# Performance work log

Hardware: AMD Instinct MI355X
Metric: run time of the kernel (lower is better)

Reference implementation:

```python
import jax, jax.numpy as jnp
import numpy as np

N, F, H, K, T, O = 4096, 64, 64, 2, 5, 32  # nodes, in_feat, hidden, heads, temporal_steps, out


def setup_inputs() -> dict:
    key = jax.random.key(0)
    ks = jax.random.split(key, 12)
    s = 0.05
    return {
        "node_features": jax.random.normal(ks[0], (N, F), jnp.float32),
        "adj_matrix": jax.random.randint(ks[1], (N, N), 0, 2, jnp.int32),
        "temporal_features": jax.random.normal(ks[2], (N, T, H), jnp.float32),
        # GAT params (stacked over K heads). Linear W: Wh = h @ W.T, so W_gat[k] is [H, F].
        "W_gat": jax.random.normal(ks[3], (K, H, F), jnp.float32) * s,
        "a_src": jax.random.normal(ks[4], (K, H), jnp.float32) * s,  # first half of a (repeat -> column/neighbor index)
        "a_dst": jax.random.normal(ks[5], (K, H), jnp.float32) * s,  # second half of a (repeat_interleave -> row/self index)
        # LSTM (1 layer, input K*H, hidden H), PyTorch gate order i,f,g,o
        "W_ih": jax.random.normal(ks[6], (4 * H, K * H), jnp.float32) * s,
        "W_hh": jax.random.normal(ks[7], (4 * H, H), jnp.float32) * s,
        "b_ih": jax.random.normal(ks[8], (4 * H,), jnp.float32) * s,
        "b_hh": jax.random.normal(ks[9], (4 * H,), jnp.float32) * s,
        # fc
        "fc_W": jax.random.normal(ks[10], (O, H), jnp.float32) * s,
        "fc_b": jax.random.normal(ks[11], (O,), jnp.float32) * s,
    }


def reference(node_features, adj_matrix, temporal_features,
              W_gat, a_src, a_dst, W_ih, W_hh, b_ih, b_hh, fc_W, fc_b):
    # ---- GAT heads (vectorized over K) ----
    Wh = jnp.einsum("nf,khf->knh", node_features, W_gat)          # [K,N,H]
    # a([Wh_i, Wh_j]) == a_src.Wh_j + a_dst.Wh_i; e[p,q] = lrelu(dst[p] + src[q])
    s_src = jnp.einsum("knh,kh->kn", Wh, a_src)                    # column term
    s_dst = jnp.einsum("knh,kh->kn", Wh, a_dst)                    # row term
    e = jax.nn.leaky_relu(s_dst[:, :, None] + s_src[:, None, :], 0.2)  # [K,N,N]
    e = jnp.where(adj_matrix[None, :, :] > 0, e, jnp.float32(-1e9))
    att = jax.nn.softmax(e, axis=-1)                               # dropout = identity (eval)
    h_prime = jax.nn.elu(jnp.einsum("kpq,kqh->kph", att, Wh))      # [K,N,H]
    h = jnp.transpose(h_prime, (1, 0, 2)).reshape(N, K * H)        # concat heads [N, K*H]
    # ---- LSTM over seq of length 1 (h.unsqueeze(1)); h0 = c0 = 0 ----
    gates = h @ W_ih.T + b_ih + b_hh                               # h0 @ W_hh.T == 0
    i, f, g, o = jnp.split(gates, 4, axis=-1)
    c = jax.nn.sigmoid(i) * jnp.tanh(g)                            # f * c0 == 0
    h_t = jax.nn.sigmoid(o) * jnp.tanh(c)                          # [N,H]
    return h_t @ fc_W.T + fc_b                                     # [N,O]
```

## Files before the change

### kernel.cpp

```cpp
#include <hip/hip_runtime.h>


#define NN 4096

typedef __attribute__((ext_vector_type(8))) short bf16x8;
typedef __attribute__((ext_vector_type(4))) float f32x4;

__device__ inline unsigned short bf_rne(float f) {
    unsigned u = __float_as_uint(f);
    u += 0x7fffu + ((u >> 16) & 1u);
    return (unsigned short)(u >> 16);
}

__device__ inline unsigned cvt_pk_bf16(float lo, float hi) {
    unsigned r;
    asm("v_cvt_pk_bf16_f32 %0, %1, %2" : "=v"(r) : "v"(lo), "v"(hi));
    return r;
}

__device__ inline float sigf(float x) { return 1.f / (1.f + __expf(-x)); }

__global__ __launch_bounds__(256) void adj2bytes(
    const int* __restrict__ adj, unsigned char* __restrict__ ab)
{
    const int tid = blockIdx.x * 256 + threadIdx.x;
    const int4* __restrict__ a4 = (const int4*)adj;
#pragma unroll
    for (int r = 0; r < 4; ++r) {
        const int idx = tid + r * 524288;
        const int4 x = a4[idx * 2];
        const int4 y = a4[idx * 2 + 1];
        unsigned b = 0;
        b |= (x.x > 0) ? 1u : 0u;  b |= (x.y > 0) ? 2u : 0u;
        b |= (x.z > 0) ? 4u : 0u;  b |= (x.w > 0) ? 8u : 0u;
        b |= (y.x > 0) ? 16u : 0u; b |= (y.y > 0) ? 32u : 0u;
        b |= (y.z > 0) ? 64u : 0u; b |= (y.w > 0) ? 128u : 0u;
        ab[idx] = (unsigned char)b;
    }
}

__global__ __launch_bounds__(256) void prep_small(
    const float* __restrict__ X, const float* __restrict__ Wg,
    const float* __restrict__ a_src, const float* __restrict__ a_dst,
    const float* __restrict__ W_ih, const float* __restrict__ b_ih,
    const float* __restrict__ b_hh, const float* __restrict__ fc_W,
    unsigned short* __restrict__ whB, float* __restrict__ e1s,
    float* __restrict__ e2s, float* __restrict__ e1d, float* __restrict__ e2d,
    unsigned short* __restrict__ Wpk, unsigned short* __restrict__ fcb,
    float* __restrict__ biasg)
{
    __shared__ float X_lds[64][64];
    __shared__ float Wh_lds[64][65];
    __shared__ float spart[64][4][2];
    const int t = threadIdx.x;
    const int bid = blockIdx.x;

    if (bid >= 64) {
        const int idx = (bid - 64) * 256 + t;
        if (idx < 24576) {
            const int j = idx & 7, lane = (idx >> 3) & 63;
            const int k0 = (idx >> 9) & 3, tt = idx >> 11;
            const int jj = tt * 16 + (lane & 15);
            const int m = k0 * 32 + (lane >> 4) * 8 + j;
            const int sr = (jj < 64) ? jj : 64 + jj;
            Wpk[idx] = bf_rne(W_ih[sr * 128 + m]);
        } else if (idx < 26624) {
            const int o = idx - 24576;
            const int j = o & 7, lane = (o >> 3) & 63;
            const int k0 = (o >> 9) & 1, tt = o >> 10;
            const int row = tt * 16 + (lane & 15);
            const int m = k0 * 32 + (lane >> 4) * 8 + j;
            fcb[o] = bf_rne(fc_W[row * 64 + m]);
        } else if (idx < 26816) {
            const int j = idx - 26624;
            const int sr = (j < 64) ? j : 64 + j;
            biasg[j] = b_ih[sr] + b_hh[sr];
        }
        return;
    }

    const int n0 = bid * 64;
#pragma unroll
    for (int i = 0; i < 16; ++i) {
        int idx = t + i * 256;
        X_lds[idx >> 6][idx & 63] = X[n0 * 64 + idx];
    }
    __syncthreads();
    const int h = t & 63, rg = t >> 6;
    for (int k = 0; k < 2; ++k) {
        float acc[16];
#pragma unroll
        for (int r = 0; r < 16; ++r) acc[r] = 0.f;
        for (int f0 = 0; f0 < 64; f0 += 4) {
            const float4 w4 = *(const float4*)&Wg[(k * 64 + h) * 64 + f0];
#pragma unroll
            for (int r = 0; r < 16; ++r) {
                const float4 x4 = *(const float4*)&X_lds[rg * 16 + r][f0];
                acc[r] += w4.x * x4.x + w4.y * x4.y + w4.z * x4.z + w4.w * x4.w;
            }
        }
        if (k) __syncthreads();
#pragma unroll
        for (int r = 0; r < 16; ++r) Wh_lds[rg * 16 + r][h] = acc[r];
        __syncthreads();
        {
            const int r = t & 63, qa = t >> 6;
            float ps = 0.f, pd = 0.f;
#pragma unroll
            for (int i = 0; i < 16; ++i) {
                const int hh = qa * 16 + i;
                const float v = Wh_lds[r][hh];
                ps += v * a_src[k * 64 + hh];
                pd += v * a_dst[k * 64 + hh];
            }
            spart[r][qa][0] = ps;
            spart[r][qa][1] = pd;
        }
        {
#pragma unroll
            for (int pid = t; pid < 512; pid += 256) {
                const int n = pid & 15, qg = (pid >> 4) & 3;
                const int qb_loc = (pid >> 6) & 1, f = pid >> 7;
                const int qb = (n0 >> 5) + qb_loc;
                unsigned pk[4];
#pragma unroll
                for (int i = 0; i < 4; ++i) {
                    const int r = qb_loc * 32 + qg * 8 + 2 * i;
                    unsigned lo = bf_rne(Wh_lds[r][f * 16 + n]);
                    unsigned hi = bf_rne(Wh_lds[r + 1][f * 16 + n]);
                    pk[i] = lo | (hi << 16);
                }
                uint4* dst = (uint4*)&whB[(((k * 4 + f) * 128 + qb) * 512) + (qg * 16 + n) * 8];
                *dst = make_uint4(pk[0], pk[1], pk[2], pk[3]);
            }
        }
        __syncthreads();
        if (t < 64) {
            float s0 = spart[t][0][0] + spart[t][1][0] + spart[t][2][0] + spart[t][3][0];
            float s1 = spart[t][0][1] + spart[t][1][1] + spart[t][2][1] + spart[t][3][1];
            e1s[k * NN + n0 + t] = __expf(s0);
            e2s[k * NN + n0 + t] = __expf(0.2f * s0);
            e1d[k * NN + n0 + t] = __expf(s1);
            e2d[k * NN + n0 + t] = __expf(0.2f * s1);
        }
    }
}

__global__ __launch_bounds__(1024) void gat_attn(
    const unsigned char* __restrict__ adjbytes,
    const unsigned short* __restrict__ whB,
    const float* __restrict__ e1s, const float* __restrict__ e2s,
    const float* __restrict__ e1d, const float* __restrict__ e2d,
    const unsigned short* __restrict__ Wpk, const unsigned short* __restrict__ fcb,
    const float* __restrict__ biasg, const float* __restrict__ fc_b,
    float* __restrict__ out)
{
    __shared__ float S_all[16][2][16][64];
    __shared__ float z_all[16][2][16];
    __shared__ unsigned char byt_lds[16 * 520 + 8];
    unsigned short* h_lds = (unsigned short*)&S_all[0][0][0][0];
    float* gate_lds = (float*)((char*)&S_all[0][0][0][0] + 4608);

    const int tid = threadIdx.x;
    const int wave = tid >> 6, lane = tid & 63;
    const int rloc = lane & 15, qg = lane >> 4;
    const int p0 = blockIdx.x * 16;
    const int p = p0 + rloc;

#pragma unroll
    for (int i = tid; i < 2048; i += 1024) {
        const int row = i >> 7, off = i & 127;
        *(unsigned*)&byt_lds[row * 520 + off * 4] =
            ((const unsigned*)adjbytes)[(p0 + row) * 128 + off];
    }
    __syncthreads();

    const float e1p0 = e1d[p], e2p0 = e2d[p];
    const float e1p1 = e1d[NN + p], e2p1 = e2d[NN + p];
    const unsigned short* __restrict__ whB_l = whB + lane * 8;

    f32x4 acc[2][4];
#pragma unroll
    for (int k = 0; k < 2; ++k)
#pragma unroll
        for (int f = 0; f < 4; ++f)
            acc[k][f] = (f32x4){0.f, 0.f, 0.f, 0.f};
    float z0 = 0.f, z1 = 0.f;

    const int qbase = wave * 256;
    for (int chunk = 0; chunk < 4; ++chunk) {
#pragma unroll
        for (int kk = 0; kk < 2; ++kk) {
            const int q0 = qbase + chunk * 64 + kk * 32 + qg * 8;
            const int qb = wave * 8 + chunk * 2 + kk;
            const unsigned byte8 =
                byt_lds[rloc * 520 + wave * 32 + chunk * 8 + kk * 4 + qg];
            const float4 qa0 = *(const float4*)(e1s + q0);
            const float4 qa1 = *(const float4*)(e1s + q0 + 4);
            const float4 qb0 = *(const float4*)(e2s + q0);
            const float4 qb1 = *(const float4*)(e2s + q0 + 4);
            const float4 qc0 = *(const float4*)(e1s + NN + q0);
            const float4 qc1 = *(const float4*)(e1s + NN + q0 + 4);
            const float4 qd0 = *(const float4*)(e2s + NN + q0);
            const float4 qd1 = *(const float4*)(e2s + NN + q0 + 4);
            const float q1v0[8] = {qa0.x, qa0.y, qa0.z, qa0.w, qa1.x, qa1.y, qa1.z, qa1.w};
            const float q2v0[8] = {qb0.x, qb0.y, qb0.z, qb0.w, qb1.x, qb1.y, qb1.z, qb1.w};
            const float q1v1[8] = {qc0.x, qc0.y, qc0.z, qc0.w, qc1.x, qc1.y, qc1.z, qc1.w};
            const float q2v1[8] = {qd0.x, qd0.y, qd0.z, qd0.w, qd1.x, qd1.y, qd1.z, qd1.w};
            float w0a[8], w1a[8];
#pragma unroll
            for (int j = 0; j < 8; ++j) {
                const bool on = (byte8 & (1u << j)) != 0u;
                const float pp0 = e1p0 * q1v0[j];
                float w0 = pp0 > 1.f ? pp0 : e2p0 * q2v0[j];
                w0 = on ? w0 : 0.f;
                z0 += w0;
                w0a[j] = w0;
                const float pp1 = e1p1 * q1v1[j];
                float w1 = pp1 > 1.f ? pp1 : e2p1 * q2v1[j];
                w1 = on ? w1 : 0.f;
                z1 += w1;
                w1a[j] = w1;
            }
            union { bf16x8 v; unsigned w[4]; } fa0, fa1;
#pragma unroll
            for (int i = 0; i < 4; ++i) {
                fa0.w[i] = cvt_pk_bf16(w0a[2 * i], w0a[2 * i + 1]);
                fa1.w[i] = cvt_pk_bf16(w1a[2 * i], w1a[2 * i + 1]);
            }
#pragma unroll
            for (int f = 0; f < 4; ++f) {
                const bf16x8 b0 = *(const bf16x8*)(whB_l + ((f * 128 + qb) << 9));
                acc[0][f] = __builtin_amdgcn_mfma_f32_16x16x32_bf16(fa0.v, b0, acc[0][f], 0, 0, 0);
                const bf16x8 b1 = *(const bf16x8*)(whB_l + (((4 + f) * 128 + qb) << 9));
                acc[1][f] = __builtin_amdgcn_mfma_f32_16x16x32_bf16(fa1.v, b1, acc[1][f], 0, 0, 0);
            }
        }
    }
    z0 += __shfl_xor(z0, 16); z0 += __shfl_xor(z0, 32);
    z1 += __shfl_xor(z1, 16); z1 += __shfl_xor(z1, 32);
    if (lane < 16) { z_all[wave][0][lane] = z0; z_all[wave][1][lane] = z1; }
#pragma unroll
    for (int k = 0; k < 2; ++k)
#pragma unroll
        for (int f = 0; f < 4; ++f)
#pragma unroll
            for (int j = 0; j < 4; ++j)
                S_all[wave][k][qg * 4 + j][f * 16 + rloc] = acc[k][f][j];
    __syncthreads();
    float vreg[2]; int vk[2], vr[2], vh[2];
#pragma unroll
    for (int i = 0; i < 2; ++i) {
        const int idx = tid + i * 1024;
        const int k = idx >> 10, rr = (idx >> 6) & 15, hh = idx & 63;
        float s = 0.f, z = 0.f;
#pragma unroll
        for (int w = 0; w < 16; ++w) {
            s += S_all[w][k][rr][hh];
            z += z_all[w][k][rr];
        }
        float v = s / z;
        vreg[i] = v > 0.f ? v : expm1f(v);
        vk[i] = k; vr[i] = rr; vh[i] = hh;
    }
    __syncthreads();
#pragma unroll
    for (int i = 0; i < 2; ++i)
        h_lds[vr[i] * 136 + vk[i] * 64 + vh[i]] = bf_rne(vreg[i]);
    __syncthreads();

    const int c = lane & 15, g4 = lane >> 4;
    if (wave < 12) {
        const int t = wave;
        f32x4 ga = (f32x4){0.f, 0.f, 0.f, 0.f};
#pragma unroll
        for (int k0 = 0; k0 < 4; ++k0) {
            const bf16x8 a = *(const bf16x8*)&h_lds[c * 136 + k0 * 32 + g4 * 8];
            const bf16x8 b = *(const bf16x8*)&Wpk[((t * 4 + k0) * 64 + lane) * 8];
            ga = __builtin_amdgcn_mfma_f32_16x16x32_bf16(a, b, ga, 0, 0, 0);
        }
        const float bb = biasg[t * 16 + c];
#pragma unroll
        for (int j = 0; j < 4; ++j)
            gate_lds[(t >> 2) * 1088 + (g4 * 4 + j) * 68 + (t & 3) * 16 + c] = ga[j] + bb;
    }
    __syncthreads();
    {
        const int n = tid >> 6, hh = tid & 63;
        const float iv = gate_lds[n * 68 + hh];
        const float gv = gate_lds[1088 + n * 68 + hh];
        const float ov = gate_lds[2176 + n * 68 + hh];
        const float cv = sigf(iv) * tanhf(gv);
        const float htv = sigf(ov) * tanhf(cv);
        __syncthreads();
        h_lds[n * 136 + hh] = bf_rne(htv);
    }
    __syncthreads();
    if (wave < 2) {
        const int t2 = wave;
        f32x4 fa = (f32x4){0.f, 0.f, 0.f, 0.f};
#pragma unroll
        for (int k0 = 0; k0 < 2; ++k0) {
            const bf16x8 a = *(const bf16x8*)&h_lds[c * 136 + k0 * 32 + g4 * 8];
            const bf16x8 b = *(const bf16x8*)&fcb[((t2 * 2 + k0) * 64 + lane) * 8];
            fa = __builtin_amdgcn_mfma_f32_16x16x32_bf16(a, b, fa, 0, 0, 0);
        }
        const float fb = fc_b[t2 * 16 + c];
#pragma unroll
        for (int j = 0; j < 4; ++j)
            out[(p0 + g4 * 4 + j) * 32 + t2 * 16 + c] = fa[j] + fb;
    }
}

extern "C" void kernel_launch(void* const* d_in, const int* in_sizes, int n_in,
                              void* d_out, int out_size, void* d_ws, size_t ws_size,
                              hipStream_t stream) {
    const float* X     = (const float*)d_in[0];
    const int*   adj   = (const int*)d_in[1];
    const float* Wg    = (const float*)d_in[3];
    const float* a_src = (const float*)d_in[4];
    const float* a_dst = (const float*)d_in[5];
    const float* W_ih  = (const float*)d_in[6];
    const float* b_ih  = (const float*)d_in[8];
    const float* b_hh  = (const float*)d_in[9];
    const float* fc_W  = (const float*)d_in[10];
    const float* fc_b  = (const float*)d_in[11];
    float* out = (float*)d_out;

    char* ws = (char*)d_ws;
    unsigned short* whB = (unsigned short*)ws;
    float* e1s = (float*)(ws + (1 << 20));
    float* e2s = (float*)(ws + (1 << 20) + (32 << 10));
    float* e1d = (float*)(ws + (1 << 20) + (64 << 10));
    float* e2d = (float*)(ws + (1 << 20) + (96 << 10));
    unsigned char* adjbytes = (unsigned char*)(ws + (1 << 20) + (128 << 10));
    char* ws2 = ws + (3 << 20) + (128 << 10);
    unsigned short* Wpk = (unsigned short*)ws2;
    unsigned short* fcb = (unsigned short*)(ws2 + (48 << 10));
    float* biasg = (float*)(ws2 + (52 << 10));

    hipLaunchKernelGGL(adj2bytes, dim3(2048), dim3(256), 0, stream,
                       adj, adjbytes);
    hipLaunchKernelGGL(prep_small, dim3(169), dim3(256), 0, stream,
                       X, Wg, a_src, a_dst, W_ih, b_ih, b_hh, fc_W,
                       whB, e1s, e2s, e1d, e2d, Wpk, fcb, biasg);
    hipLaunchKernelGGL(gat_attn, dim3(256), dim3(1024), 0, stream,
                       adjbytes, whB, e1s, e2s, e1d, e2d, Wpk, fcb, biasg, fc_b, out);
}
```

Measured before the change: 56.99 us.

## Fuse adjacency bitmask packing into attention kernel with double-buffered prefetch

Removes the separate adj2bytes kernel and its byte-mask round-trip through global memory. The attention kernel now reads the int32 adjacency rows itself, packs 16 entries into a bitmask per lane, and stores them in a double-buffered LDS tile. The next chunk's loads are issued while MFMA work runs on the current one. It also reorders which columns each wave covers so that one row's mask is produced per wave, at the cost of extra block-wide barriers inside the main loop.

```diff
diff --git a/kernel.cpp b/kernel.cpp
--- a/kernel.cpp
+++ b/kernel.cpp
@@ -20,23 +20,18 @@
 
 __device__ inline float sigf(float x) { return 1.f / (1.f + __expf(-x)); }
 
-__global__ __launch_bounds__(256) void adj2bytes(
-    const int* __restrict__ adj, unsigned char* __restrict__ ab)
-{
-    const int tid = blockIdx.x * 256 + threadIdx.x;
-    const int4* __restrict__ a4 = (const int4*)adj;
-#pragma unroll
-    for (int r = 0; r < 4; ++r) {
-        const int idx = tid + r * 524288;
-        const int4 x = a4[idx * 2];
-        const int4 y = a4[idx * 2 + 1];
-        unsigned b = 0;
-        b |= (x.x > 0) ? 1u : 0u;  b |= (x.y > 0) ? 2u : 0u;
-        b |= (x.z > 0) ? 4u : 0u;  b |= (x.w > 0) ? 8u : 0u;
-        b |= (y.x > 0) ? 16u : 0u; b |= (y.y > 0) ? 32u : 0u;
-        b |= (y.z > 0) ? 64u : 0u; b |= (y.w > 0) ? 128u : 0u;
-        ab[idx] = (unsigned char)b;
-    }
+__device__ inline unsigned pack16(const int4 a, const int4 b,
+                                  const int4 c, const int4 d) {
+    unsigned m = 0;
+    m |= (a.x > 0) ? 0x0001u : 0u; m |= (a.y > 0) ? 0x0002u : 0u;
+    m |= (a.z > 0) ? 0x0004u : 0u; m |= (a.w > 0) ? 0x0008u : 0u;
+    m |= (b.x > 0) ? 0x0010u : 0u; m |= (b.y > 0) ? 0x0020u : 0u;
+    m |= (b.z > 0) ? 0x0040u : 0u; m |= (b.w > 0) ? 0x0080u : 0u;
+    m |= (c.x > 0) ? 0x0100u : 0u; m |= (c.y > 0) ? 0x0200u : 0u;
+    m |= (c.z > 0) ? 0x0400u : 0u; m |= (c.w > 0) ? 0x0800u : 0u;
+    m |= (d.x > 0) ? 0x1000u : 0u; m |= (d.y > 0) ? 0x2000u : 0u;
+    m |= (d.z > 0) ? 0x4000u : 0u; m |= (d.w > 0) ? 0x8000u : 0u;
+    return m;
 }
 
 __global__ __launch_bounds__(256) void prep_small(
@@ -147,7 +142,7 @@
 }
 
 __global__ __launch_bounds__(1024) void gat_attn(
-    const unsigned char* __restrict__ adjbytes,
+    const int* __restrict__ adj,
     const unsigned short* __restrict__ whB,
     const float* __restrict__ e1s, const float* __restrict__ e2s,
     const float* __restrict__ e1d, const float* __restrict__ e2d,
@@ -157,7 +152,7 @@
 {
     __shared__ float S_all[16][2][16][64];
     __shared__ float z_all[16][2][16];
-    __shared__ unsigned char byt_lds[16 * 520 + 8];
+    __shared__ unsigned short msk_lds[2][16][66];
     unsigned short* h_lds = (unsigned short*)&S_all[0][0][0][0];
     float* gate_lds = (float*)((char*)&S_all[0][0][0][0] + 4608);
 
@@ -167,13 +162,7 @@
     const int p0 = blockIdx.x * 16;
     const int p = p0 + rloc;
 
-#pragma unroll
-    for (int i = tid; i < 2048; i += 1024) {
-        const int row = i >> 7, off = i & 127;
-        *(unsigned*)&byt_lds[row * 520 + off * 4] =
-            ((const unsigned*)adjbytes)[(p0 + row) * 128 + off];
-    }
-    __syncthreads();
+    const int4* __restrict__ arow = (const int4*)(adj + (long)(p0 + wave) * NN);
 
     const float e1p0 = e1d[p], e2p0 = e2d[p];
     const float e1p1 = e1d[NN + p], e2p1 = e2d[NN + p];
@@ -187,14 +176,31 @@
             acc[k][f] = (f32x4){0.f, 0.f, 0.f, 0.f};
     float z0 = 0.f, z1 = 0.f;
 
-    const int qbase = wave * 256;
-    for (int chunk = 0; chunk < 4; ++chunk) {
+    {
+        const int4 a0 = arow[lane * 4 + 0];
+        const int4 a1 = arow[lane * 4 + 1];
+        const int4 a2 = arow[lane * 4 + 2];
+        const int4 a3 = arow[lane * 4 + 3];
+        msk_lds[0][wave][lane] = (unsigned short)pack16(a0, a1, a2, a3);
+    }
+    __syncthreads();
+
+#pragma unroll
+    for (int c = 0; c < 4; ++c) {
+        int4 n0v, n1v, n2v, n3v;
+        if (c < 3) {
+            const int base = (c + 1) * 256 + lane * 4;
+            n0v = arow[base + 0];
+            n1v = arow[base + 1];
+            n2v = arow[base + 2];
+            n3v = arow[base + 3];
+        }
 #pragma unroll
         for (int kk = 0; kk < 2; ++kk) {
-            const int q0 = qbase + chunk * 64 + kk * 32 + qg * 8;
-            const int qb = wave * 8 + chunk * 2 + kk;
-            const unsigned byte8 =
-                byt_lds[rloc * 520 + wave * 32 + chunk * 8 + kk * 4 + qg];
+            const int q0 = c * 1024 + wave * 64 + kk * 32 + qg * 8;
+            const int qb = c * 32 + wave * 2 + kk;
+            const unsigned mm = msk_lds[c & 1][rloc][wave * 4 + kk * 2 + (qg >> 1)];
+            const unsigned byte8 = (mm >> ((qg & 1) * 8)) & 0xffu;
             const float4 qa0 = *(const float4*)(e1s + q0);
             const float4 qa1 = *(const float4*)(e1s + q0 + 4);
             const float4 qb0 = *(const float4*)(e2s + q0);
@@ -236,6 +242,11 @@
                 acc[1][f] = __builtin_amdgcn_mfma_f32_16x16x32_bf16(fa1.v, b1, acc[1][f], 0, 0, 0);
             }
         }
+        if (c < 3) {
+            msk_lds[(c + 1) & 1][wave][lane] =
+                (unsigned short)pack16(n0v, n1v, n2v, n3v);
+            __syncthreads();
+        }
     }
     z0 += __shfl_xor(z0, 16); z0 += __shfl_xor(z0, 32);
     z1 += __shfl_xor(z1, 16); z1 += __shfl_xor(z1, 32);
@@ -269,20 +280,20 @@
         h_lds[vr[i] * 136 + vk[i] * 64 + vh[i]] = bf_rne(vreg[i]);
     __syncthreads();
 
-    const int c = lane & 15, g4 = lane >> 4;
+    const int c2 = lane & 15, g4 = lane >> 4;
     if (wave < 12) {
         const int t = wave;
         f32x4 ga = (f32x4){0.f, 0.f, 0.f, 0.f};
 #pragma unroll
         for (int k0 = 0; k0 < 4; ++k0) {
-            const bf16x8 a = *(const bf16x8*)&h_lds[c * 136 + k0 * 32 + g4 * 8];
+            const bf16x8 a = *(const bf16x8*)&h_lds[c2 * 136 + k0 * 32 + g4 * 8];
             const bf16x8 b = *(const bf16x8*)&Wpk[((t * 4 + k0) * 64 + lane) * 8];
             ga = __builtin_amdgcn_mfma_f32_16x16x32_bf16(a, b, ga, 0, 0, 0);
         }
-        const float bb = biasg[t * 16 + c];
+        const float bb = biasg[t * 16 + c2];
 #pragma unroll
         for (int j = 0; j < 4; ++j)
-            gate_lds[(t >> 2) * 1088 + (g4 * 4 + j) * 68 + (t & 3) * 16 + c] = ga[j] + bb;
+            gate_lds[(t >> 2) * 1088 + (g4 * 4 + j) * 68 + (t & 3) * 16 + c2] = ga[j] + bb;
     }
     __syncthreads();
     {
@@ -301,14 +312,14 @@
         f32x4 fa = (f32x4){0.f, 0.f, 0.f, 0.f};
 #pragma unroll
         for (int k0 = 0; k0 < 2; ++k0) {
-            const bf16x8 a = *(const bf16x8*)&h_lds[c * 136 + k0 * 32 + g4 * 8];
+            const bf16x8 a = *(const bf16x8*)&h_lds[c2 * 136 + k0 * 32 + g4 * 8];
             const bf16x8 b = *(const bf16x8*)&fcb[((t2 * 2 + k0) * 64 + lane) * 8];
             fa = __builtin_amdgcn_mfma_f32_16x16x32_bf16(a, b, fa, 0, 0, 0);
         }
-        const float fb = fc_b[t2 * 16 + c];
+        const float fb = fc_b[t2 * 16 + c2];
 #pragma unroll
         for (int j = 0; j < 4; ++j)
-            out[(p0 + g4 * 4 + j) * 32 + t2 * 16 + c] = fa[j] + fb;
+            out[(p0 + g4 * 4 + j) * 32 + t2 * 16 + c2] = fa[j] + fb;
     }
 }
 
@@ -333,17 +344,14 @@
     float* e2s = (float*)(ws + (1 << 20) + (32 << 10));
     float* e1d = (float*)(ws + (1 << 20) + (64 << 10));
     float* e2d = (float*)(ws + (1 << 20) + (96 << 10));
-    unsigned char* adjbytes = (unsigned char*)(ws + (1 << 20) + (128 << 10));
-    char* ws2 = ws + (3 << 20) + (128 << 10);
+    char* ws2 = ws + (1 << 20) + (128 << 10);
     unsigned short* Wpk = (unsigned short*)ws2;
     unsigned short* fcb = (unsigned short*)(ws2 + (48 << 10));
     float* biasg = (float*)(ws2 + (52 << 10));
 
-    hipLaunchKernelGGL(adj2bytes, dim3(2048), dim3(256), 0, stream,
-                       adj, adjbytes);
     hipLaunchKernelGGL(prep_small, dim3(169), dim3(256), 0, stream,
                        X, Wg, a_src, a_dst, W_ih, b_ih, b_hh, fc_W,
                        whB, e1s, e2s, e1d, e2d, Wpk, fcb, biasg);
     hipLaunchKernelGGL(gat_attn, dim3(256), dim3(1024), 0, stream,
-                       adjbytes, whB, e1s, e2s, e1d, e2d, Wpk, fcb, biasg, fc_b, out);
-}
+                       adj, whB, e1s, e2s, e1d, e2d, Wpk, fcb, biasg, fc_b, out);
+}
```

Measured after the change: 58.38 us. 1.02x slower.
